# Performance work log

Hardware: AMD Instinct MI355X
Metric: run time of the kernel (lower is better)

Reference implementation:

```python
import jax, jax.numpy as jnp
import numpy as np

H = 2048        # hidden_nodes
T = 8192        # timeseries length
WASHOUT = 200
SPECTRAL_RADIUS = 0.9


def setup_inputs() -> dict:
    key = jax.random.key(0)
    k1, k2, k3 = jax.random.split(key, 3)
    u = jax.random.normal(k1, (T,), dtype=jnp.float32)
    # w_res ~ uniform(-0.5, 0.5), rescaled to approximate spectral radius 0.9
    w_res = jax.random.uniform(k2, (H, H), dtype=jnp.float32) - 0.5
    unif_std = 1.0 / np.sqrt(12.0)
    w_res = w_res * np.float32(SPECTRAL_RADIUS / (unif_std * np.sqrt(H)))
    # w_in ~ uniform(-0.5, 0.5) * input_scaling(=1.0)
    w_in = jax.random.uniform(k3, (H,), dtype=jnp.float32) - 0.5
    w_out = jnp.ones((H,), dtype=jnp.float32)
    # w_out_density = 1.0 -> mask covers all nodes (identity gather)
    w_out_mask = jnp.arange(H, dtype=jnp.int32)
    return {"u": u, "w_res": w_res, "w_in": w_in, "w_out": w_out,
            "w_out_mask": w_out_mask, "washout": WASHOUT}


def reference(u, w_res, w_in, w_out, w_out_mask, washout):
    # Inference path (y=None, awgn_test_std=0, adc_quantization=None):
    #   x_{t} = tanh(w_in * u_t + w_res @ x_{t-1}); X[t] = x_t[mask]
    #   return X[washout:] @ w_out
    def step(x, u_t):
        x = jnp.tanh(w_in * u_t + w_res @ x)   # [H]
        return x, x[w_out_mask]                # carry, per-step readout row

    x0 = jnp.zeros((w_res.shape[0],), dtype=u.dtype)
    _, X = jax.lax.scan(step, x0, u)           # X: [T, output_dim]
    return X[washout:] @ w_out                 # [T - washout]
```

## Files before the change

### kernel.cpp

```cpp
#include <hip/hip_runtime.h>
#include <math.h>


#define H_   2048
#define RPB  8
#define NBLK 256
typedef unsigned long long ull;

__global__ void esn_zero(float* __restrict__ p, int n)
{
    int i = blockIdx.x * blockDim.x + threadIdx.x;
    int stride = gridDim.x * blockDim.x;
    for (; i < n; i += stride) p[i] = 0.0f;
}

__global__ __launch_bounds__(1024) void esn_scatter_c(const int* __restrict__ mask,
                                                      const float* __restrict__ w_out,
                                                      float* __restrict__ ws_f, int H)
{
    float* c = ws_f + 8192;
    for (int i = threadIdx.x; i < H; i += blockDim.x)
        atomicAdd(&c[mask[i]], w_out[i]);
}

__global__ __launch_bounds__(256) void esn_run(const float* __restrict__ u,
                                               const float* __restrict__ w_res,
                                               const float* __restrict__ w_in,
                                               float* __restrict__ out,
                                               float* __restrict__ ws_f,
                                               int T, int washout, int use_part)
{
    __shared__ float Wlds[RPB * H_];
    __shared__ float xs[H_];
    __shared__ float psum[4];

    const int tid  = threadIdx.x;
    const int wave = tid >> 6;
    const int lane = tid & 63;
    const int bid  = blockIdx.x;
    const int r0 = 2 * wave, r1 = 2 * wave + 1;
    const int grow0 = bid * RPB + r0, grow1 = bid * RPB + r1;

    {
        const float4* src = (const float4*)(w_res + (size_t)bid * RPB * H_);
        float4* dst = (float4*)Wlds;
        for (int i = tid; i < RPB * H_ / 4; i += 256) dst[i] = src[i];
    }
    float win0 = 0.f, win1 = 0.f, c0 = 0.f, c1 = 0.f;
    if (lane == 0) {
        win0 = w_in[grow0]; win1 = w_in[grow1];
        c0 = ws_f[8192 + grow0]; c1 = ws_f[8192 + grow1];
    }

    ull* pairs = (ull*)ws_f;
    float* part = ws_f + 10240;

    const float4* w0p = (const float4*)(Wlds + r0 * H_);
    const float4* w1p = (const float4*)(Wlds + (r0 + 1) * H_);
    const float4* xs4 = (const float4*)xs;

    float u_next = u[0];
    __syncthreads();

    for (int k = 0; k < T; ++k) {
        const ull* sp = pairs + (k & 1) * H_;
        ull*       dp = pairs + ((k + 1) & 1) * H_;
        float uk = u_next;
        if (k + 1 < T) u_next = u[k + 1];

        ull pv[8];
#pragma unroll
        for (int i = 0; i < 8; ++i)
            pv[i] = __hip_atomic_load(sp + (i << 8) + tid, __ATOMIC_RELAXED,
                                      __HIP_MEMORY_SCOPE_AGENT);
        {
            int spins = 0;
            for (;;) {
                unsigned pend = 0;
#pragma unroll
                for (int i = 0; i < 8; ++i)
                    if ((unsigned)(pv[i] >> 32) != (unsigned)k) {
                        pv[i] = __hip_atomic_load(sp + (i << 8) + tid,
                                                  __ATOMIC_RELAXED,
                                                  __HIP_MEMORY_SCOPE_AGENT);
                        pend = 1;
                    }
                if (!pend) break;
                if (++spins > 500000) break;
            }
        }
#pragma unroll
        for (int i = 0; i < 8; ++i)
            xs[(i << 8) + tid] = __uint_as_float((unsigned)pv[i]);
        __syncthreads();

        float4 a0 = {0.f,0.f,0.f,0.f}, a1 = {0.f,0.f,0.f,0.f};
#pragma unroll
        for (int c = 0; c < 8; ++c) {
            float4 xv  = xs4[c * 64 + lane];
            float4 wv0 = w0p[c * 64 + lane];
            float4 wv1 = w1p[c * 64 + lane];
            a0.x = fmaf(wv0.x, xv.x, a0.x); a0.y = fmaf(wv0.y, xv.y, a0.y);
            a0.z = fmaf(wv0.z, xv.z, a0.z); a0.w = fmaf(wv0.w, xv.w, a0.w);
            a1.x = fmaf(wv1.x, xv.x, a1.x); a1.y = fmaf(wv1.y, xv.y, a1.y);
            a1.z = fmaf(wv1.z, xv.z, a1.z); a1.w = fmaf(wv1.w, xv.w, a1.w);
        }
        float s0 = (a0.x + a0.y) + (a0.z + a0.w);
        float s1 = (a1.x + a1.y) + (a1.z + a1.w);
#pragma unroll
        for (int d = 1; d < 64; d <<= 1) {
            s0 += __shfl_xor(s0, d);
            s1 += __shfl_xor(s1, d);
        }

        if (lane == 0) {
            float z0 = fmaf(win0, uk, s0);
            float z1 = fmaf(win1, uk, s1);
            z0 = fminf(fmaxf(z0, -15.f), 15.f);
            z1 = fminf(fmaxf(z1, -15.f), 15.f);
            float e0 = __expf(2.f * z0), e1 = __expf(2.f * z1);
            float t0 = (e0 - 1.f) / (e0 + 1.f), t1 = (e1 - 1.f) / (e1 + 1.f);
            ull p0 = ((ull)(unsigned)(k + 1) << 32) | (ull)__float_as_uint(t0);
            ull p1 = ((ull)(unsigned)(k + 1) << 32) | (ull)__float_as_uint(t1);
            (void)__hip_atomic_exchange(dp + grow0, p0, __ATOMIC_RELAXED,
                                        __HIP_MEMORY_SCOPE_AGENT);
            (void)__hip_atomic_exchange(dp + grow1, p1, __ATOMIC_RELAXED,
                                        __HIP_MEMORY_SCOPE_AGENT);
            psum[wave] = c0 * t0 + c1 * t1;
        }
        __syncthreads();

        if (tid == 0) {
            float pw = (psum[0] + psum[1]) + (psum[2] + psum[3]);
            if (use_part) part[(size_t)k * NBLK + bid] = pw;
            else if (k >= washout) atomicAdd(&out[k - washout], pw);
        }
    }
}

__global__ __launch_bounds__(256) void esn_reduce(const float* __restrict__ part,
                                                  float* __restrict__ out,
                                                  int out_size, int washout)
{
    int wv = threadIdx.x >> 6, lane = threadIdx.x & 63;
    int t = blockIdx.x * 4 + wv;
    if (t >= out_size) return;
    const float4* p = (const float4*)(part + (size_t)(t + washout) * NBLK);
    float4 v = p[lane];
    float s = (v.x + v.y) + (v.z + v.w);
#pragma unroll
    for (int d = 1; d < 64; d <<= 1) s += __shfl_xor(s, d);
    if (lane == 0) out[t] = s;
}

extern "C" void kernel_launch(void* const* d_in, const int* in_sizes, int n_in,
                              void* d_out, int out_size, void* d_ws, size_t ws_size,
                              hipStream_t stream)
{
    const float* u     = (const float*)d_in[0];
    const float* w_res = (const float*)d_in[1];
    const float* w_in  = (const float*)d_in[2];
    const float* w_out = (const float*)d_in[3];
    const int*   mask  = (const int*)d_in[4];
    int T = in_sizes[0];
    int H = in_sizes[2];
    int washout = T - out_size;
    float* out  = (float*)d_out;
    float* ws_f = (float*)d_ws;

    size_t need = (size_t)(10240 + (size_t)T * NBLK) * 4;
    int use_part = (ws_size >= need) ? 1 : 0;

    hipLaunchKernelGGL(esn_zero, dim3(64), dim3(256), 0, stream, ws_f, 10240);
    if (!use_part)
        hipLaunchKernelGGL(esn_zero, dim3(32), dim3(256), 0, stream, out, out_size);
    hipLaunchKernelGGL(esn_scatter_c, dim3(1), dim3(1024), 0, stream, mask, w_out, ws_f, H);

    void* args[] = { (void*)&u, (void*)&w_res, (void*)&w_in, (void*)&out,
                     (void*)&ws_f, (void*)&T, (void*)&washout, (void*)&use_part };
    hipError_t e = hipLaunchCooperativeKernel((const void*)esn_run,
                                              dim3(NBLK), dim3(256),
                                              args, 0, stream);
    if (e != hipSuccess) {
        hipLaunchKernelGGL(esn_run, dim3(NBLK), dim3(256), 0, stream,
                           u, w_res, w_in, out, ws_f, T, washout, use_part);
    }
    if (use_part)
        hipLaunchKernelGGL(esn_reduce, dim3((out_size + 3) / 4), dim3(256), 0, stream,
                           ws_f + 10240, out, out_size, washout);
}
```

Baseline: 33.32 ms.

## Replace per-element tagged state words with per-block flags and packed state values

Each element of the state exchange used to carry a step tag in a 64-bit word, and every consumer polled all of them. Now each block writes its two outputs as one packed 64-bit word, then publishes a single per-block step flag after a waitcnt and barrier. Consumers spin on one flag per thread and then load four packed words. This halves the traffic for state data and cuts the number of polled locations. The risk is that relaxed atomics and a waitcnt now have to order the data writes before the flag write at agent scope.

```diff
diff --git a/kernel.cpp b/kernel.cpp
--- a/kernel.cpp
+++ b/kernel.cpp
@@ -38,8 +38,8 @@
     const int wave = tid >> 6;
     const int lane = tid & 63;
     const int bid  = blockIdx.x;
-    const int r0 = 2 * wave, r1 = 2 * wave + 1;
-    const int grow0 = bid * RPB + r0, grow1 = bid * RPB + r1;
+    const int r0 = 2 * wave;
+    const int grow0 = bid * RPB + r0, grow1 = grow0 + 1;
 
     {
         const float4* src = (const float4*)(w_res + (size_t)bid * RPB * H_);
@@ -52,58 +52,66 @@
         c0 = ws_f[8192 + grow0]; c1 = ws_f[8192 + grow1];
     }
 
-    ull* pairs = (ull*)ws_f;
+    ull*          xv = (ull*)ws_f;
+    unsigned int* fl = (unsigned int*)(ws_f + 4096);
     float* part = ws_f + 10240;
 
     const float4* w0p = (const float4*)(Wlds + r0 * H_);
     const float4* w1p = (const float4*)(Wlds + (r0 + 1) * H_);
     const float4* xs4 = (const float4*)xs;
+    float4* xs4w = (float4*)xs;
 
     float u_next = u[0];
     __syncthreads();
 
     for (int k = 0; k < T; ++k) {
-        const ull* sp = pairs + (k & 1) * H_;
-        ull*       dp = pairs + ((k + 1) & 1) * H_;
+        const ull*    sp = xv + (k & 1) * 1024 + 4 * tid;
+        ull*          dp = xv + ((k + 1) & 1) * 1024;
+        unsigned int* sf = fl + (k & 1) * 256;
+        unsigned int* df = fl + ((k + 1) & 1) * 256;
         float uk = u_next;
         if (k + 1 < T) u_next = u[k + 1];
 
-        ull pv[8];
-#pragma unroll
-        for (int i = 0; i < 8; ++i)
-            pv[i] = __hip_atomic_load(sp + (i << 8) + tid, __ATOMIC_RELAXED,
-                                      __HIP_MEMORY_SCOPE_AGENT);
         {
             int spins = 0;
             for (;;) {
-                unsigned pend = 0;
-#pragma unroll
-                for (int i = 0; i < 8; ++i)
-                    if ((unsigned)(pv[i] >> 32) != (unsigned)k) {
-                        pv[i] = __hip_atomic_load(sp + (i << 8) + tid,
-                                                  __ATOMIC_RELAXED,
-                                                  __HIP_MEMORY_SCOPE_AGENT);
-                        pend = 1;
-                    }
-                if (!pend) break;
+                unsigned int f = __hip_atomic_load(sf + tid, __ATOMIC_RELAXED,
+                                                   __HIP_MEMORY_SCOPE_AGENT);
+                if (f == (unsigned int)k) break;
                 if (++spins > 500000) break;
             }
         }
-#pragma unroll
-        for (int i = 0; i < 8; ++i)
-            xs[(i << 8) + tid] = __uint_as_float((unsigned)pv[i]);
+        __builtin_amdgcn_sched_barrier(0);
+
+        {
+            ull v0 = __hip_atomic_load(sp + 0, __ATOMIC_RELAXED, __HIP_MEMORY_SCOPE_AGENT);
+            ull v1 = __hip_atomic_load(sp + 1, __ATOMIC_RELAXED, __HIP_MEMORY_SCOPE_AGENT);
+            ull v2 = __hip_atomic_load(sp + 2, __ATOMIC_RELAXED, __HIP_MEMORY_SCOPE_AGENT);
+            ull v3 = __hip_atomic_load(sp + 3, __ATOMIC_RELAXED, __HIP_MEMORY_SCOPE_AGENT);
+            float4 a, b;
+            a.x = __uint_as_float((unsigned int)v0);
+            a.y = __uint_as_float((unsigned int)(v0 >> 32));
+            a.z = __uint_as_float((unsigned int)v1);
+            a.w = __uint_as_float((unsigned int)(v1 >> 32));
+            b.x = __uint_as_float((unsigned int)v2);
+            b.y = __uint_as_float((unsigned int)(v2 >> 32));
+            b.z = __uint_as_float((unsigned int)v3);
+            b.w = __uint_as_float((unsigned int)(v3 >> 32));
+            xs4w[2 * tid]     = a;
+            xs4w[2 * tid + 1] = b;
+        }
         __syncthreads();
 
         float4 a0 = {0.f,0.f,0.f,0.f}, a1 = {0.f,0.f,0.f,0.f};
 #pragma unroll
         for (int c = 0; c < 8; ++c) {
-            float4 xv  = xs4[c * 64 + lane];
+            float4 xvv = xs4[c * 64 + lane];
             float4 wv0 = w0p[c * 64 + lane];
             float4 wv1 = w1p[c * 64 + lane];
-            a0.x = fmaf(wv0.x, xv.x, a0.x); a0.y = fmaf(wv0.y, xv.y, a0.y);
-            a0.z = fmaf(wv0.z, xv.z, a0.z); a0.w = fmaf(wv0.w, xv.w, a0.w);
-            a1.x = fmaf(wv1.x, xv.x, a1.x); a1.y = fmaf(wv1.y, xv.y, a1.y);
-            a1.z = fmaf(wv1.z, xv.z, a1.z); a1.w = fmaf(wv1.w, xv.w, a1.w);
+            a0.x = fmaf(wv0.x, xvv.x, a0.x); a0.y = fmaf(wv0.y, xvv.y, a0.y);
+            a0.z = fmaf(wv0.z, xvv.z, a0.z); a0.w = fmaf(wv0.w, xvv.w, a0.w);
+            a1.x = fmaf(wv1.x, xvv.x, a1.x); a1.y = fmaf(wv1.y, xvv.y, a1.y);
+            a1.z = fmaf(wv1.z, xvv.z, a1.z); a1.w = fmaf(wv1.w, xvv.w, a1.w);
         }
         float s0 = (a0.x + a0.y) + (a0.z + a0.w);
         float s1 = (a1.x + a1.y) + (a1.z + a1.w);
@@ -120,17 +128,17 @@
             z1 = fminf(fmaxf(z1, -15.f), 15.f);
             float e0 = __expf(2.f * z0), e1 = __expf(2.f * z1);
             float t0 = (e0 - 1.f) / (e0 + 1.f), t1 = (e1 - 1.f) / (e1 + 1.f);
-            ull p0 = ((ull)(unsigned)(k + 1) << 32) | (ull)__float_as_uint(t0);
-            ull p1 = ((ull)(unsigned)(k + 1) << 32) | (ull)__float_as_uint(t1);
-            (void)__hip_atomic_exchange(dp + grow0, p0, __ATOMIC_RELAXED,
-                                        __HIP_MEMORY_SCOPE_AGENT);
-            (void)__hip_atomic_exchange(dp + grow1, p1, __ATOMIC_RELAXED,
-                                        __HIP_MEMORY_SCOPE_AGENT);
+            ull p01 = (ull)__float_as_uint(t0) | ((ull)__float_as_uint(t1) << 32);
+            (void)__hip_atomic_exchange(dp + (bid * 4 + wave), p01,
+                                        __ATOMIC_RELAXED, __HIP_MEMORY_SCOPE_AGENT);
             psum[wave] = c0 * t0 + c1 * t1;
         }
+        asm volatile("s_waitcnt vmcnt(0)" ::: "memory");
         __syncthreads();
 
         if (tid == 0) {
+            (void)__hip_atomic_exchange(df + bid, (unsigned int)(k + 1),
+                                        __ATOMIC_RELAXED, __HIP_MEMORY_SCOPE_AGENT);
             float pw = (psum[0] + psum[1]) + (psum[2] + psum[3]);
             if (use_part) part[(size_t)k * NBLK + bid] = pw;
             else if (k >= washout) atomicAdd(&out[k - washout], pw);
```

After: 47.65 ms. +43.0%, slower.

## Replicate the per-step state broadcast buffer into eight copies to spread polling

Applied to the files above, without the earlier changes.

Each block now writes its new state values into eight replicated double-buffered arrays, using eight lanes, and each block polls only the replica chosen by its block index. The goal is to cut contention from all 256 blocks spin-reading the same cache lines every timestep. In exchange every step does eight times more atomic writes, and the workspace layout offsets grow to hold the replicas.

```diff
diff --git a/kernel.cpp b/kernel.cpp
--- a/kernel.cpp
+++ b/kernel.cpp
@@ -5,6 +5,7 @@
 #define H_   2048
 #define RPB  8
 #define NBLK 256
+#define NREP 8
 typedef unsigned long long ull;
 
 __global__ void esn_zero(float* __restrict__ p, int n)
@@ -18,7 +19,7 @@
                                                       const float* __restrict__ w_out,
                                                       float* __restrict__ ws_f, int H)
 {
-    float* c = ws_f + 8192;
+    float* c = ws_f + 65536;
     for (int i = threadIdx.x; i < H; i += blockDim.x)
         atomicAdd(&c[mask[i]], w_out[i]);
 }
@@ -38,8 +39,8 @@
     const int wave = tid >> 6;
     const int lane = tid & 63;
     const int bid  = blockIdx.x;
-    const int r0 = 2 * wave, r1 = 2 * wave + 1;
-    const int grow0 = bid * RPB + r0, grow1 = bid * RPB + r1;
+    const int r0 = 2 * wave;
+    const int grow0 = bid * RPB + r0, grow1 = grow0 + 1;
 
     {
         const float4* src = (const float4*)(w_res + (size_t)bid * RPB * H_);
@@ -49,22 +50,23 @@
     float win0 = 0.f, win1 = 0.f, c0 = 0.f, c1 = 0.f;
     if (lane == 0) {
         win0 = w_in[grow0]; win1 = w_in[grow1];
-        c0 = ws_f[8192 + grow0]; c1 = ws_f[8192 + grow1];
+        c0 = ws_f[65536 + grow0]; c1 = ws_f[65536 + grow1];
     }
 
-    ull* pairs = (ull*)ws_f;
-    float* part = ws_f + 10240;
+    ull* xv = (ull*)ws_f;
+    float* part = ws_f + 67584;
 
     const float4* w0p = (const float4*)(Wlds + r0 * H_);
     const float4* w1p = (const float4*)(Wlds + (r0 + 1) * H_);
     const float4* xs4 = (const float4*)xs;
 
+    const ull* rbase = xv + (size_t)(bid & (NREP - 1)) * 4096;
+
     float u_next = u[0];
     __syncthreads();
 
     for (int k = 0; k < T; ++k) {
-        const ull* sp = pairs + (k & 1) * H_;
-        ull*       dp = pairs + ((k + 1) & 1) * H_;
+        const ull* sp = rbase + (k & 1) * 2048;
         float uk = u_next;
         if (k + 1 < T) u_next = u[k + 1];
 
@@ -97,13 +99,13 @@
         float4 a0 = {0.f,0.f,0.f,0.f}, a1 = {0.f,0.f,0.f,0.f};
 #pragma unroll
         for (int c = 0; c < 8; ++c) {
-            float4 xv  = xs4[c * 64 + lane];
+            float4 xvv = xs4[c * 64 + lane];
             float4 wv0 = w0p[c * 64 + lane];
             float4 wv1 = w1p[c * 64 + lane];
-            a0.x = fmaf(wv0.x, xv.x, a0.x); a0.y = fmaf(wv0.y, xv.y, a0.y);
-            a0.z = fmaf(wv0.z, xv.z, a0.z); a0.w = fmaf(wv0.w, xv.w, a0.w);
-            a1.x = fmaf(wv1.x, xv.x, a1.x); a1.y = fmaf(wv1.y, xv.y, a1.y);
-            a1.z = fmaf(wv1.z, xv.z, a1.z); a1.w = fmaf(wv1.w, xv.w, a1.w);
+            a0.x = fmaf(wv0.x, xvv.x, a0.x); a0.y = fmaf(wv0.y, xvv.y, a0.y);
+            a0.z = fmaf(wv0.z, xvv.z, a0.z); a0.w = fmaf(wv0.w, xvv.w, a0.w);
+            a1.x = fmaf(wv1.x, xvv.x, a1.x); a1.y = fmaf(wv1.y, xvv.y, a1.y);
+            a1.z = fmaf(wv1.z, xvv.z, a1.z); a1.w = fmaf(wv1.w, xvv.w, a1.w);
         }
         float s0 = (a0.x + a0.y) + (a0.z + a0.w);
         float s1 = (a1.x + a1.y) + (a1.z + a1.w);
@@ -113,6 +115,7 @@
             s1 += __shfl_xor(s1, d);
         }
 
+        ull p0 = 0, p1 = 0;
         if (lane == 0) {
             float z0 = fmaf(win0, uk, s0);
             float z1 = fmaf(win1, uk, s1);
@@ -120,13 +123,18 @@
             z1 = fminf(fmaxf(z1, -15.f), 15.f);
             float e0 = __expf(2.f * z0), e1 = __expf(2.f * z1);
             float t0 = (e0 - 1.f) / (e0 + 1.f), t1 = (e1 - 1.f) / (e1 + 1.f);
-            ull p0 = ((ull)(unsigned)(k + 1) << 32) | (ull)__float_as_uint(t0);
-            ull p1 = ((ull)(unsigned)(k + 1) << 32) | (ull)__float_as_uint(t1);
-            (void)__hip_atomic_exchange(dp + grow0, p0, __ATOMIC_RELAXED,
+            p0 = ((ull)(unsigned)(k + 1) << 32) | (ull)__float_as_uint(t0);
+            p1 = ((ull)(unsigned)(k + 1) << 32) | (ull)__float_as_uint(t1);
+            psum[wave] = c0 * t0 + c1 * t1;
+        }
+        p0 = __shfl(p0, 0, 64);
+        p1 = __shfl(p1, 0, 64);
+        if (lane < NREP) {
+            ull* dpr = xv + (size_t)lane * 4096 + ((k + 1) & 1) * 2048;
+            (void)__hip_atomic_exchange(dpr + grow0, p0, __ATOMIC_RELAXED,
                                         __HIP_MEMORY_SCOPE_AGENT);
-            (void)__hip_atomic_exchange(dp + grow1, p1, __ATOMIC_RELAXED,
+            (void)__hip_atomic_exchange(dpr + grow1, p1, __ATOMIC_RELAXED,
                                         __HIP_MEMORY_SCOPE_AGENT);
-            psum[wave] = c0 * t0 + c1 * t1;
         }
         __syncthreads();
 
@@ -168,10 +176,10 @@
     float* out  = (float*)d_out;
     float* ws_f = (float*)d_ws;
 
-    size_t need = (size_t)(10240 + (size_t)T * NBLK) * 4;
+    size_t need = (size_t)(67584 + (size_t)T * NBLK) * 4;
     int use_part = (ws_size >= need) ? 1 : 0;
 
-    hipLaunchKernelGGL(esn_zero, dim3(64), dim3(256), 0, stream, ws_f, 10240);
+    hipLaunchKernelGGL(esn_zero, dim3(128), dim3(256), 0, stream, ws_f, 67584);
     if (!use_part)
         hipLaunchKernelGGL(esn_zero, dim3(32), dim3(256), 0, stream, out, out_size);
     hipLaunchKernelGGL(esn_scatter_c, dim3(1), dim3(1024), 0, stream, mask, w_out, ws_f, H);
@@ -187,5 +195,5 @@
     }
     if (use_part)
         hipLaunchKernelGGL(esn_reduce, dim3((out_size + 3) / 4), dim3(256), 0, stream,
-                           ws_f + 10240, out, out_size, washout);
+                           ws_f + 67584, out, out_size, washout);
 }
```

Result: no change. 32.88 ms (median of 2 runs) (-1.3%).
